# Optimization experiments

Measured on AMD Instinct MI355X. Metric: run time of the kernel, lower is better.

Reference implementation:

```python
import jax, jax.numpy as jnp
import numpy as np

B, C, L = 32, 64, 4096
HIDDEN = 64
SR = 50.0
KS = (7, 15, 31, 63)
PHYS = 12
EPS_BN = 1e-5
EPS_GN = 1e-5


def _dwconv(x, w):
    # x: (B,C,L), w: (C,1,k) depthwise kernel, SAME padding for odd k
    k = w.shape[-1]
    p = (k - 1) // 2
    return jax.lax.conv_general_dilated(
        x, w, window_strides=(1,), padding=[(p, p)],
        dimension_numbers=('NCH', 'OIH', 'NCH'),
        feature_group_count=x.shape[1])


def _physics(x):
    b, c, l = x.shape
    svm = jnp.sqrt((x * x).sum(axis=1))                      # (B,L) channel norm
    svm_max = svm.max(axis=-1)
    svm_mean = svm.mean(axis=-1)
    svm_std = jnp.std(svm, axis=-1, ddof=1) + 1e-6           # torch.std is unbiased
    jerk = jnp.diff(x, axis=-1) * SR                         # (B,C,L-1)
    jerk_max = jnp.abs(jerk).max(axis=-1).mean(axis=-1)      # (B,)
    jerk_rate = jnp.diff(jerk, axis=-1) * SR
    jerk_rate_max = jnp.abs(jerk_rate).max(axis=-1).mean(axis=-1)
    sign_changes = (x[:, :, :-1] * x[:, :, 1:] < 0).astype(x.dtype)
    zcr = sign_changes.sum(axis=-1).mean(axis=-1) / l
    thr = (svm_mean + 2.0 * svm_std)[:, None]
    impact_duration = (svm > thr).astype(x.dtype).sum(axis=-1) / l
    hthr = (svm_mean + 3.0 * svm_std)[:, None]
    impact_ratio = (svm > hthr).astype(x.dtype).sum(axis=-1) / l
    free_fall = (svm < (svm_mean - svm_std)[:, None]).astype(x.dtype).sum(axis=-1) / l
    second_half = svm[:, l // 2:]
    post_stillness = jnp.tanh(1.0 / (jnp.std(second_half, axis=-1, ddof=1) + 1e-6))
    third = max(1, l // 3)
    pre_mean = svm[:, :third].mean(axis=-1)
    impact_peak = svm[:, third:2 * third].max(axis=-1)
    post_mean = svm[:, 2 * third:].mean(axis=-1)
    fall_phase = jax.nn.relu(impact_peak - pre_mean) + jax.nn.relu(impact_peak - post_mean)
    fall_phase = fall_phase / (jnp.abs(impact_peak) + 1e-6)
    spectrum = jnp.fft.rfft(x.astype(jnp.float32), axis=-1, norm='ortho')
    power = (jnp.abs(spectrum) ** 2).sum(axis=1)             # (B, L//2+1)
    freqs = jnp.linspace(0.0, 1.0, power.shape[-1], dtype=power.dtype)
    total_power = power.sum(axis=-1) + 1e-6
    spectral_centroid = (power * freqs).sum(axis=-1) / total_power
    high_freq_ratio = jnp.where(freqs > 0.4, power, 0.0).sum(axis=-1) / total_power
    feats = jnp.stack([svm_max, svm_mean, jerk_max, jerk_rate_max, zcr,
                       impact_duration, impact_ratio, post_stillness, free_fall,
                       spectral_centroid, high_freq_ratio, fall_phase], axis=-1)
    return jnp.nan_to_num(feats, nan=0.0, posinf=0.0, neginf=0.0).astype(x.dtype)


def _forward(x, dw_w7, dw_w15, dw_w31, dw_w63, bn_g, bn_b, bn_m, bn_v,
             comp_w1, comp_b1, comp_w2, comp_b2,
             pn_g, pn_b, pn_m, pn_v,
             pe_w1, pe_b1, pe_w2, pe_b2, pg_w, pg_b,
             temperature, gn_g, gn_b, proj_w, proj_b, res_scale):
    # 4 depthwise conv + BN(eval) branches
    branches = []
    for i, w in enumerate((dw_w7, dw_w15, dw_w31, dw_w63)):
        y = _dwconv(x, w)
        y = (y - bn_m[i][None, :, None]) / jnp.sqrt(bn_v[i][None, :, None] + EPS_BN) \
            * bn_g[i][None, :, None] + bn_b[i][None, :, None]
        branches.append(y)
    stacked = jnp.stack(branches, axis=1)                    # (B,4,C,L)
    # complexity net: global avg pool -> MLP
    xm = x.mean(axis=-1)                                     # (B,C)
    h = jax.nn.relu(xm @ comp_w1 + comp_b1)
    complexity_logits = h @ comp_w2 + comp_b2                # (B,4)
    # physics gate
    pf = _physics(x)                                         # (B,12)
    pf = (pf - pn_m) / jnp.sqrt(pn_v + EPS_BN) * pn_g + pn_b
    pe = jax.nn.relu(jax.nn.relu(pf @ pe_w1 + pe_b1) @ pe_w2 + pe_b2)
    physics_weights = jax.nn.sigmoid(pe @ pg_w + pg_b)       # (B,4)
    temp = jnp.maximum(temperature, 0.1)
    weights = jax.nn.softmax(complexity_logits * physics_weights / temp, axis=-1)
    mixed = jnp.einsum('bkcl,bk->bcl', stacked, weights)
    # proj: GroupNorm(1,C) -> GELU(exact) -> 1x1 conv
    mu = mixed.mean(axis=(1, 2), keepdims=True)
    var = mixed.var(axis=(1, 2), keepdims=True)
    gn = (mixed - mu) / jnp.sqrt(var + EPS_GN) * gn_g[None, :, None] + gn_b[None, :, None]
    act = jax.nn.gelu(gn, approximate=False)
    out = jnp.einsum('oc,bcl->bol', proj_w, act) + proj_b[None, :, None]
    return x + res_scale * out


def setup_inputs() -> dict:
    ks = jax.random.split(jax.random.key(0), 16)
    f32 = jnp.float32
    inp = {}
    inp['x'] = jax.random.normal(ks[0], (B, C, L), dtype=f32)
    for i, k in enumerate(KS):
        inp[f'dw_w{k}'] = jax.random.normal(ks[1 + i], (C, 1, k), dtype=f32) / np.sqrt(k)
    inp['bn_g'] = jnp.ones((4, C), f32)
    inp['bn_b'] = jnp.zeros((4, C), f32)
    inp['bn_m'] = 0.1 * jax.random.normal(ks[5], (4, C), dtype=f32)
    inp['bn_v'] = jax.random.uniform(ks[6], (4, C), dtype=f32, minval=0.5, maxval=1.5)
    inp['comp_w1'] = jax.random.normal(ks[7], (C, HIDDEN), dtype=f32) / np.sqrt(C)
    inp['comp_b1'] = jnp.zeros((HIDDEN,), f32)
    inp['comp_w2'] = jax.random.normal(ks[8], (HIDDEN, 4), dtype=f32) / np.sqrt(HIDDEN)
    inp['comp_b2'] = jnp.zeros((4,), f32)
    inp['pn_g'] = jnp.ones((PHYS,), f32)
    inp['pn_b'] = jnp.zeros((PHYS,), f32)
    inp['pn_m'] = 0.1 * jax.random.normal(ks[9], (PHYS,), dtype=f32)
    inp['pn_v'] = jax.random.uniform(ks[10], (PHYS,), dtype=f32, minval=0.5, maxval=1.5)
    inp['pe_w1'] = jax.random.normal(ks[11], (PHYS, 32), dtype=f32) / np.sqrt(PHYS)
    inp['pe_b1'] = jnp.zeros((32,), f32)
    inp['pe_w2'] = jax.random.normal(ks[12], (32, 32), dtype=f32) / np.sqrt(32)
    inp['pe_b2'] = jnp.zeros((32,), f32)
    inp['pg_w'] = jax.random.normal(ks[13], (32, 4), dtype=f32) / np.sqrt(32)
    inp['pg_b'] = jnp.zeros((4,), f32)
    inp['temperature'] = jnp.asarray(1.0, f32)
    inp['gn_g'] = jnp.ones((C,), f32)
    inp['gn_b'] = jnp.zeros((C,), f32)
    inp['proj_w'] = jax.random.normal(ks[14], (C, C), dtype=f32) / np.sqrt(C)
    inp['proj_b'] = jnp.zeros((C,), f32)
    inp['res_scale'] = jnp.asarray(0.5, f32)  # init is 0.0; 0.5 gives a non-trivial output
    return inp


def reference(x, dw_w7, dw_w15, dw_w31, dw_w63, bn_g, bn_b, bn_m, bn_v,
              comp_w1, comp_b1, comp_w2, comp_b2,
              pn_g, pn_b, pn_m, pn_v,
              pe_w1, pe_b1, pe_w2, pe_b2, pg_w, pg_b,
              temperature, gn_g, gn_b, proj_w, proj_b, res_scale):
    return _forward(x, dw_w7, dw_w15, dw_w31, dw_w63, bn_g, bn_b, bn_m, bn_v,
                    comp_w1, comp_b1, comp_w2, comp_b2, pn_g, pn_b, pn_m, pn_v,
                    pe_w1, pe_b1, pe_w2, pe_b2, pg_w, pg_b,
                    temperature, gn_g, gn_b, proj_w, proj_b, res_scale)
```

## Files before the change

kernel.cpp:

```cpp
#include <hip/hip_runtime.h>
#include <math.h>

#define LN 4096
#define CN 64
#define BQ 32
#define NTH 256

#define OFF_CHAN_SUM    0
#define OFF_CHAN_JERK   2048
#define OFF_CHAN_JRATE  4096
#define OFF_CHAN_ZCR    6144
#define OFF_SVMST_PART  8192
#define OFF_SPEC_PART   12288
#define OFF_EFF_B       15360
#define OFF_GNP         17408
#define OFF_EFF_W       21504
#define OFF_SVMBUF      152576

#define FP(i) ((i) + ((i) >> 4))

__device__ __forceinline__ void bfly4(float2& a, float2& b, float2& c, float2& d,
                                      float w1r, float w1i, float w2r, float w2i,
                                      float w3r, float w3i) {
  float t1r = b.x*w1r - b.y*w1i, t1i = b.x*w1i + b.y*w1r;
  float t2r = c.x*w2r - c.y*w2i, t2i = c.x*w2i + c.y*w2r;
  float t3r = d.x*w3r - d.y*w3i, t3i = d.x*w3i + d.y*w3r;
  float ar = a.x + t2r, ai = a.y + t2i;
  float br = a.x - t2r, bi = a.y - t2i;
  float cr = t1r + t3r, ci = t1i + t3i;
  float dr = t1r - t3r, di = t1i - t3i;
  a = make_float2(ar + cr, ai + ci);
  b = make_float2(br + di, bi - dr);
  c = make_float2(ar - cr, ai - ci);
  d = make_float2(br - di, bi + dr);
}

__global__ __launch_bounds__(NTH) void kS(const float* __restrict__ x, float* __restrict__ ws) {
  __shared__ __align__(16) char smraw[34880];
  int role = blockIdx.x;
  int t = threadIdx.x;

  if (role < 2048) {
    int bc = role;
    const float* row = x + (size_t)bc * LN;
    int l0 = t * 16;
    float rd[18];
    const float4* r4 = (const float4*)(row + l0);
#pragma unroll
    for (int q = 0; q < 4; q++) {
      float4 v = r4[q];
      rd[4*q] = v.x; rd[4*q+1] = v.y; rd[4*q+2] = v.z; rd[4*q+3] = v.w;
    }
    if (t < 255) { rd[16] = row[l0 + 16]; rd[17] = row[l0 + 17]; }
    else { rd[16] = 0.f; rd[17] = 0.f; }
    float lsum = 0.f, jm = 0.f, jrm = 0.f; int zc = 0;
#pragma unroll
    for (int i = 0; i < 16; i++) {
      float a = rd[i], b2 = rd[i+1];
      lsum += a;
      int l = l0 + i;
      if (l < LN - 1) {
        jm = fmaxf(jm, fabsf(b2 - a));
        zc += (a * b2 < 0.f);
        if (l < LN - 2) jrm = fmaxf(jrm, fabsf(rd[i+2] - 2.f*b2 + a));
      }
    }
    for (int off = 32; off > 0; off >>= 1) {
      lsum += __shfl_down(lsum, off);
      jm = fmaxf(jm, __shfl_down(jm, off));
      jrm = fmaxf(jrm, __shfl_down(jrm, off));
      zc += __shfl_down(zc, off);
    }
    float* s1 = (float*)smraw; float* s2_ = s1 + 4; float* s3 = s1 + 8; int* s4 = (int*)(s1 + 12);
    int w = t >> 6;
    if ((t & 63) == 0) { s1[w] = lsum; s2_[w] = jm; s3[w] = jrm; s4[w] = zc; }
    __syncthreads();
    if (t == 0) {
      float S = 0, J = 0, JR = 0; int Z = 0;
      for (int i = 0; i < 4; i++) { S += s1[i]; J = fmaxf(J, s2_[i]); JR = fmaxf(JR, s3[i]); Z += s4[i]; }
      ws[OFF_CHAN_SUM + bc]   = S;
      ws[OFF_CHAN_JERK + bc]  = J * 50.f;
      ws[OFF_CHAN_JRATE + bc] = JR * 2500.f;
      ws[OFF_CHAN_ZCR + bc]   = (float)Z;
    }
  } else if (role < 2560) {
    int blk = role - 2048;
    int b = blk >> 4, lt = blk & 15;
    int l = lt * 256 + t;
    const float* xb = x + (size_t)b * CN * LN + l;
    float acc = 0.f;
#pragma unroll
    for (int c = 0; c < CN; c++) { float v = xb[(size_t)c * LN]; acc = fmaf(v, v, acc); }
    float svm = sqrtf(acc);
    ws[OFF_SVMBUF + (size_t)b * LN + l] = svm;
    const int third = LN / 3;
    float vS = svm, vS2 = svm * svm;
    float vS2H  = (l >= LN/2) ? svm : 0.f;
    float vS2H2 = (l >= LN/2) ? svm * svm : 0.f;
    float vPRE  = (l < third) ? svm : 0.f;
    float vPOST = (l >= 2*third) ? svm : 0.f;
    float vMX = svm;
    float vMID = (l >= third && l < 2*third) ? svm : 0.f;
    for (int off = 32; off > 0; off >>= 1) {
      vS += __shfl_down(vS, off); vS2 += __shfl_down(vS2, off);
      vS2H += __shfl_down(vS2H, off); vS2H2 += __shfl_down(vS2H2, off);
      vPRE += __shfl_down(vPRE, off); vPOST += __shfl_down(vPOST, off);
      vMX = fmaxf(vMX, __shfl_down(vMX, off));
      vMID = fmaxf(vMID, __shfl_down(vMID, off));
    }
    float (*red)[4] = (float(*)[4])smraw;
    int w = t >> 6;
    if ((t & 63) == 0) {
      red[0][w] = vS; red[1][w] = vS2; red[2][w] = vMX; red[3][w] = vS2H;
      red[4][w] = vS2H2; red[5][w] = vPRE; red[6][w] = vMID; red[7][w] = vPOST;
    }
    __syncthreads();
    if (t == 0) {
      float* sp = ws + OFF_SVMST_PART + (size_t)blk * 8;
      sp[0] = red[0][0]+red[0][1]+red[0][2]+red[0][3];
      sp[1] = red[1][0]+red[1][1]+red[1][2]+red[1][3];
      sp[2] = fmaxf(fmaxf(red[2][0],red[2][1]),fmaxf(red[2][2],red[2][3]));
      sp[3] = red[3][0]+red[3][1]+red[3][2]+red[3][3];
      sp[4] = red[4][0]+red[4][1]+red[4][2]+red[4][3];
      sp[5] = red[5][0]+red[5][1]+red[5][2]+red[5][3];
      sp[6] = fmaxf(fmaxf(red[6][0],red[6][1]),fmaxf(red[6][2],red[6][3]));
      sp[7] = red[7][0]+red[7][1]+red[7][2]+red[7][3];
    }
  } else {
    int blk = role - 2560;
    int b = blk >> 5, cp = blk & 31;
    const float* r0 = x + ((size_t)b * CN + 2 * cp) * LN;
    const float* r1 = r0 + LN;
    float2* z = (float2*)smraw;
    float (*red)[4] = (float(*)[4])(smraw + 34816);
#pragma unroll
    for (int k = 0; k < 4; k++) {
      int n4 = (k * 256 + t) * 4;
      float4 a = *(const float4*)(r0 + n4);
      float4 c = *(const float4*)(r1 + n4);
      float ar[4] = {a.x, a.y, a.z, a.w}, cr[4] = {c.x, c.y, c.z, c.w};
#pragma unroll
      for (int q = 0; q < 4; q++) {
        unsigned n = (unsigned)(n4 + q);
        unsigned br = __brev(n) >> 20;
        unsigned dr = ((br & 0x555u) << 1) | ((br & 0xAAAu) >> 1);
        z[FP(dr)] = make_float2(ar[q], cr[q]);
      }
    }
    __syncthreads();
    const float c8r[4] = { 1.f, 0.92387953251f, 0.70710678119f, 0.38268343236f };
    const float c8i[4] = { 0.f, -0.38268343236f, -0.70710678119f, -0.92387953251f };
#pragma unroll
    for (int p = 0; p < 3; p++) {
      const int H = (p == 0) ? 1 : (p == 1) ? 16 : 256;
      int r = t & (H - 1);
      int B = ((t / H) * 16 * H) + r;
      float2 E[16];
#pragma unroll
      for (int q = 0; q < 16; q++) E[q] = z[FP(B + q * H)];
      float su, cu;
      sincospif((float)r / (8.0f * (float)H), &su, &cu);
      float ur = cu, ui = -su;
      float u2r = ur*ur - ui*ui, u2i = 2.f*ur*ui;
      float w1r = u2r*u2r - u2i*u2i, w1i = 2.f*u2r*u2i;
      float w2r = w1r*w1r - w1i*w1i, w2i = 2.f*w1r*w1i;
      float w3r = w2r*w1r - w2i*w1i, w3i = w2r*w1i + w2i*w1r;
#pragma unroll
      for (int m = 0; m < 4; m++)
        bfly4(E[4*m], E[4*m+1], E[4*m+2], E[4*m+3], w1r, w1i, w2r, w2i, w3r, w3i);
#pragma unroll
      for (int m = 0; m < 4; m++) {
        float W1r = ur*c8r[m] - ui*c8i[m];
        float W1i = ur*c8i[m] + ui*c8r[m];
        float W2r = W1r*W1r - W1i*W1i, W2i = 2.f*W1r*W1i;
        float W3r = W2r*W1r - W2i*W1i, W3i = W2r*W1i + W2i*W1r;
        bfly4(E[m], E[m+4], E[m+8], E[m+12], W1r, W1i, W2r, W2i, W3r, W3i);
      }
#pragma unroll
      for (int q = 0; q < 16; q++) z[FP(B + q * H)] = E[q];
      __syncthreads();
    }
    float tot = 0.f, cen = 0.f, hi = 0.f;
    for (int k = t; k <= LN / 2; k += NTH) {
      float p;
      if (k == 0 || k == LN / 2) {
        float2 v = z[FP(k)];
        p = v.x * v.x + v.y * v.y;
      } else {
        float2 zk = z[FP(k)], zn = z[FP(LN - k)];
        float a1 = zk.x + zn.x, a2 = zk.y - zn.y, a3 = zk.y + zn.y, a4 = zk.x - zn.x;
        p = 0.25f * (a1*a1 + a2*a2 + a3*a3 + a4*a4);
      }
      p *= (1.0f / LN);
      tot += p;
      cen += p * ((float)k * (1.0f / (LN / 2)));
      if (k >= 820) hi += p;
    }
    for (int off = 32; off > 0; off >>= 1) {
      tot += __shfl_down(tot, off);
      cen += __shfl_down(cen, off);
      hi  += __shfl_down(hi, off);
    }
    int w = t >> 6;
    if ((t & 63) == 0) { red[0][w] = tot; red[1][w] = cen; red[2][w] = hi; }
    __syncthreads();
    if (t == 0) {
      float* sp = ws + OFF_SPEC_PART + (size_t)blk * 3;
      sp[0] = red[0][0]+red[0][1]+red[0][2]+red[0][3];
      sp[1] = red[1][0]+red[1][1]+red[1][2]+red[1][3];
      sp[2] = red[2][0]+red[2][1]+red[2][2]+red[2][3];
    }
  }
}

__global__ __launch_bounds__(NTH) void k4_gate(
    const float* __restrict__ dw7, const float* __restrict__ dw15,
    const float* __restrict__ dw31, const float* __restrict__ dw63,
    const float* __restrict__ bn_g, const float* __restrict__ bn_b,
    const float* __restrict__ bn_m, const float* __restrict__ bn_v,
    const float* __restrict__ comp_w1, const float* __restrict__ comp_b1,
    const float* __restrict__ comp_w2, const float* __restrict__ comp_b2,
    const float* __restrict__ pn_g, const float* __restrict__ pn_b,
    const float* __restrict__ pn_m, const float* __restrict__ pn_v,
    const float* __restrict__ pe_w1, const float* __restrict__ pe_b1,
    const float* __restrict__ pe_w2, const float* __restrict__ pe_b2,
    const float* __restrict__ pg_w, const float* __restrict__ pg_b,
    const float* __restrict__ temperature,
    float* __restrict__ ws)
{
  int b = blockIdx.x, t = threadIdx.x;
  __shared__ float sp8[16][8];
  __shared__ float sp3[32][3];
  __shared__ float stv[10];
  __shared__ float bc2[2];
  __shared__ float xm[64], h[64], pf[12], pe1v[32], pe2v[32], lgts[4], wts[4];
  __shared__ int ri[3][4], cnts[3];
  if (t < 16) {
    const float* p = ws + OFF_SVMST_PART + (size_t)(b * 16 + t) * 8;
#pragma unroll
    for (int i = 0; i < 8; i++) sp8[t][i] = p[i];
  }
  if (t >= 32 && t < 64) {
    int i = t - 32;
    const float* p = ws + OFF_SPEC_PART + (size_t)(b * 32 + i) * 3;
    sp3[i][0] = p[0]; sp3[i][1] = p[1]; sp3[i][2] = p[2];
  }
  __syncthreads();
  if (t == 0) {
    float S=0,S2=0,MX=-1e30f,S2H=0,S2H2=0,PRE=0,MID=-1e30f,POST=0;
    for (int i = 0; i < 16; i++) {
      S += sp8[i][0]; S2 += sp8[i][1]; MX = fmaxf(MX, sp8[i][2]);
      S2H += sp8[i][3]; S2H2 += sp8[i][4]; PRE += sp8[i][5];
      MID = fmaxf(MID, sp8[i][6]); POST += sp8[i][7];
    }
    float tot=0,cen=0,hi=0;
    for (int i = 0; i < 32; i++) { tot += sp3[i][0]; cen += sp3[i][1]; hi += sp3[i][2]; }
    stv[0]=S; stv[1]=S2; stv[2]=MX; stv[3]=S2H; stv[4]=S2H2;
    stv[5]=PRE; stv[6]=MID; stv[7]=POST; stv[8]=cen/(tot+1e-6f); stv[9]=hi/(tot+1e-6f);
    float mean = S * (1.f / LN);
    float var = (S2 - S * S * (1.f / LN)) * (1.f / (LN - 1));
    var = fmaxf(var, 0.f);
    bc2[0] = mean;
    bc2[1] = sqrtf(var) + 1e-6f;
  }
  __syncthreads();
  float mean = bc2[0], stde = bc2[1];
  float thr2 = mean + 2.f * stde, thr3 = mean + 3.f * stde, thrf = mean - stde;
  const float* svm = ws + OFF_SVMBUF + (size_t)b * LN;
  int c2 = 0, c3 = 0, cf = 0;
  for (int l = t; l < LN; l += NTH) {
    float v = svm[l];
    c2 += (v > thr2); c3 += (v > thr3); cf += (v < thrf);
  }
  for (int off = 32; off > 0; off >>= 1) {
    c2 += __shfl_down(c2, off); c3 += __shfl_down(c3, off); cf += __shfl_down(cf, off);
  }
  int w = t >> 6;
  if ((t & 63) == 0) { ri[0][w] = c2; ri[1][w] = c3; ri[2][w] = cf; }
  float j = 0.f, jr = 0.f, zz = 0.f;
  if (t < 64) {
    xm[t] = ws[OFF_CHAN_SUM + b * 64 + t] * (1.0f / LN);
    j  = ws[OFF_CHAN_JERK + b * 64 + t];
    jr = ws[OFF_CHAN_JRATE + b * 64 + t];
    zz = ws[OFF_CHAN_ZCR + b * 64 + t];
    for (int off = 32; off > 0; off >>= 1) {
      j += __shfl_down(j, off); jr += __shfl_down(jr, off); zz += __shfl_down(zz, off);
    }
  }
  __syncthreads();
  if (t == 0) {
    cnts[0] = ri[0][0]+ri[0][1]+ri[0][2]+ri[0][3];
    cnts[1] = ri[1][0]+ri[1][1]+ri[1][2]+ri[1][3];
    cnts[2] = ri[2][0]+ri[2][1]+ri[2][2]+ri[2][3];
    const int third = LN / 3;
    float S2H = stv[3], S2H2 = stv[4];
    float n2 = (float)(LN / 2);
    float var2 = (S2H2 - S2H * S2H / n2) / (n2 - 1.f);
    var2 = fmaxf(var2, 0.f);
    float post_still = tanhf(1.f / (sqrtf(var2) + 1e-6f));
    float pre_mean = stv[5] / (float)third;
    float post_mean = stv[7] / (float)(LN - 2 * third);
    float pk = stv[6];
    float fp = fmaxf(pk - pre_mean, 0.f) + fmaxf(pk - post_mean, 0.f);
    fp = fp / (fabsf(pk) + 1e-6f);
    pf[0] = stv[2];
    pf[1] = mean;
    pf[2] = j * (1.f / 64);
    pf[3] = jr * (1.f / 64);
    pf[4] = (zz * (1.f / 64)) * (1.f / LN);
    pf[5] = (float)cnts[0] / LN;
    pf[6] = (float)cnts[1] / LN;
    pf[7] = post_still;
    pf[8] = (float)cnts[2] / LN;
    pf[9] = stv[8];
    pf[10] = stv[9];
    pf[11] = fp;
  }
  __syncthreads();
  if (t < 12) pf[t] = (pf[t] - pn_m[t]) * rsqrtf(pn_v[t] + 1e-5f) * pn_g[t] + pn_b[t];
  __syncthreads();
  if (t < 64) {
    float hv = comp_b1[t];
    for (int i = 0; i < 64; i++) hv = fmaf(xm[i], comp_w1[i * 64 + t], hv);
    h[t] = fmaxf(hv, 0.f);
  }
  if (t < 32) {
    float v = pe_b1[t];
    for (int i = 0; i < 12; i++) v = fmaf(pf[i], pe_w1[i * 32 + t], v);
    pe1v[t] = fmaxf(v, 0.f);
  }
  __syncthreads();
  if (t < 32) {
    float v = pe_b2[t];
    for (int i = 0; i < 32; i++) v = fmaf(pe1v[i], pe_w2[i * 32 + t], v);
    pe2v[t] = fmaxf(v, 0.f);
  }
  __syncthreads();
  if (t < 4) {
    float v = comp_b2[t];
    for (int i = 0; i < 64; i++) v = fmaf(h[i], comp_w2[i * 4 + t], v);
    float g = pg_b[t];
    for (int i = 0; i < 32; i++) g = fmaf(pe2v[i], pg_w[i * 4 + t], g);
    g = 1.f / (1.f + expf(-g));
    float temp = fmaxf(temperature[0], 0.1f);
    lgts[t] = v * g / temp;
  }
  __syncthreads();
  if (t < 4) {
    float m = fmaxf(fmaxf(lgts[0], lgts[1]), fmaxf(lgts[2], lgts[3]));
    float den = expf(lgts[0]-m) + expf(lgts[1]-m) + expf(lgts[2]-m) + expf(lgts[3]-m);
    wts[t] = expf(lgts[t] - m) / den;
  }
  __syncthreads();
  if (t < 64) {
    int c = t;
    float w0 = wts[0], w1 = wts[1], w2 = wts[2], w3 = wts[3];
    float sc0 = bn_g[0*64+c] * rsqrtf(bn_v[0*64+c] + 1e-5f);
    float sc1 = bn_g[1*64+c] * rsqrtf(bn_v[1*64+c] + 1e-5f);
    float sc2 = bn_g[2*64+c] * rsqrtf(bn_v[2*64+c] + 1e-5f);
    float sc3 = bn_g[3*64+c] * rsqrtf(bn_v[3*64+c] + 1e-5f);
    float o0 = bn_b[0*64+c] - bn_m[0*64+c] * sc0;
    float o1 = bn_b[1*64+c] - bn_m[1*64+c] * sc1;
    float o2 = bn_b[2*64+c] - bn_m[2*64+c] * sc2;
    float o3 = bn_b[3*64+c] - bn_m[3*64+c] * sc3;
    ws[OFF_EFF_B + b * 64 + c] = w0*o0 + w1*o1 + w2*o2 + w3*o3;
    float a0 = w0*sc0, a1 = w1*sc1, a2 = w2*sc2, a3 = w3*sc3;
    float* eff = ws + OFF_EFF_W + (size_t)(b * 64 + c) * 64;
    for (int tau = 0; tau < 64; tau++) {
      float v = 0.f;
      if (tau < 63) {
        v = a3 * dw63[c * 63 + tau];
        int i7 = tau - 28;  if (i7 >= 0 && i7 < 7)   v = fmaf(a0, dw7[c * 7 + i7], v);
        int i15 = tau - 24; if (i15 >= 0 && i15 < 15) v = fmaf(a1, dw15[c * 15 + i15], v);
        int i31 = tau - 16; if (i31 >= 0 && i31 < 31) v = fmaf(a2, dw31[c * 31 + i31], v);
      }
      eff[tau] = v;
    }
  }
}

__device__ __forceinline__ float4 ldmask(const float* __restrict__ row, int idx) {
  int idxc = idx < 0 ? 0 : (idx > LN - 4 ? LN - 4 : idx);
  float4 v = *(const float4*)(row + idxc);
  float m = (idx == idxc) ? 1.f : 0.f;
  v.x *= m; v.y *= m; v.z *= m; v.w *= m;
  return v;
}

#define F16(wv,a0,a1,a2,a3,a4,a5,a6,a7,a8,a9,aA,aB,aC,aD,aE,aF) \
  acc[0]=fmaf(wv,a0,acc[0]);  acc[1]=fmaf(wv,a1,acc[1]);  acc[2]=fmaf(wv,a2,acc[2]);  acc[3]=fmaf(wv,a3,acc[3]);  \
  acc[4]=fmaf(wv,a4,acc[4]);  acc[5]=fmaf(wv,a5,acc[5]);  acc[6]=fmaf(wv,a6,acc[6]);  acc[7]=fmaf(wv,a7,acc[7]);  \
  acc[8]=fmaf(wv,a8,acc[8]);  acc[9]=fmaf(wv,a9,acc[9]);  acc[10]=fmaf(wv,aA,acc[10]); acc[11]=fmaf(wv,aB,acc[11]); \
  acc[12]=fmaf(wv,aC,acc[12]); acc[13]=fmaf(wv,aD,acc[13]); acc[14]=fmaf(wv,aE,acc[14]); acc[15]=fmaf(wv,aF,acc[15]);

__global__ __launch_bounds__(NTH) void k5_conv(const float* __restrict__ x,
                                               float* __restrict__ ws,
                                               float* __restrict__ mixed_out) {
  int bc = blockIdx.x;
  int t = threadIdx.x;
  __shared__ float wt[64];
  __shared__ float biasS;
  __shared__ double rda[2][4];
  if (t < 64) wt[t] = ws[OFF_EFF_W + (size_t)bc * 64 + t];
  if (t == 0) biasS = ws[OFF_EFF_B + bc];
  const float* row = x + (size_t)bc * LN;
  int l0 = t * 16;
  int g0 = l0 - 32;
  float4 R0 = ldmask(row, g0);
  float4 R1 = ldmask(row, g0 + 4);
  float4 R2 = ldmask(row, g0 + 8);
  float4 R3 = ldmask(row, g0 + 12);
  float4 R4 = ldmask(row, g0 + 16);
  __syncthreads();
  float bias = biasS;
  float acc[16];
#pragma unroll
  for (int jj = 0; jj < 16; jj++) acc[jj] = bias;
#pragma unroll
  for (int g = 0; g < 16; g++) {
    float w0 = wt[4*g], w1 = wt[4*g+1], w2 = wt[4*g+2], w3 = wt[4*g+3];
    F16(w0, R0.y,R0.z,R0.w,R1.x,R1.y,R1.z,R1.w,R2.x,R2.y,R2.z,R2.w,R3.x,R3.y,R3.z,R3.w,R4.x)
    F16(w1, R0.z,R0.w,R1.x,R1.y,R1.z,R1.w,R2.x,R2.y,R2.z,R2.w,R3.x,R3.y,R3.z,R3.w,R4.x,R4.y)
    F16(w2, R0.w,R1.x,R1.y,R1.z,R1.w,R2.x,R2.y,R2.z,R2.w,R3.x,R3.y,R3.z,R3.w,R4.x,R4.y,R4.z)
    F16(w3, R1.x,R1.y,R1.z,R1.w,R2.x,R2.y,R2.z,R2.w,R3.x,R3.y,R3.z,R3.w,R4.x,R4.y,R4.z,R4.w)
    if (g < 15) {
      R0 = R1; R1 = R2; R2 = R3; R3 = R4;
      R4 = ldmask(row, g0 + 4 * (g + 5));
    }
  }
  double ls = 0, ls2 = 0;
#pragma unroll
  for (int jj = 0; jj < 16; jj++) { float v = acc[jj]; ls += v; ls2 += (double)v * (double)v; }
  for (int off = 32; off > 0; off >>= 1) {
    ls += __shfl_down(ls, off);
    ls2 += __shfl_down(ls2, off);
  }
  int w = t >> 6;
  if ((t & 63) == 0) { rda[0][w] = ls; rda[1][w] = ls2; }
  __syncthreads();
  if (t == 0) {
    double* gp = (double*)(ws + OFF_GNP);
    gp[2 * bc + 0] = rda[0][0]+rda[0][1]+rda[0][2]+rda[0][3];
    gp[2 * bc + 1] = rda[1][0]+rda[1][1]+rda[1][2]+rda[1][3];
  }
  float* dst = mixed_out + (size_t)bc * LN + l0;
#pragma unroll
  for (int q = 0; q < 4; q++) {
    float4 v; v.x = acc[4*q]; v.y = acc[4*q+1]; v.z = acc[4*q+2]; v.w = acc[4*q+3];
    *(float4*)(dst + 4 * q) = v;
  }
}

__global__ __launch_bounds__(NTH) void k6_final(const float* __restrict__ x,
    const float* __restrict__ proj_w, const float* __restrict__ proj_b,
    const float* __restrict__ gn_g, const float* __restrict__ gn_b,
    const float* __restrict__ res_scale,
    const float* __restrict__ ws, float* out) {
  int blk = blockIdx.x;
  int b = blk >> 5;
  int l0 = (blk & 31) * 128;
  __shared__ float actS[64 * 128];
  __shared__ float Wt[64 * 64];
  __shared__ double rg[2][4];
  __shared__ float bcst[2];
  int t = threadIdx.x;
  {
    const double* gp = (const double*)(ws + OFF_GNP) + (size_t)b * CN * 2;
    double s1 = 0, s2 = 0;
    for (int i = t; i < CN; i += NTH) { s1 += gp[2*i]; s2 += gp[2*i+1]; }
    for (int off = 32; off > 0; off >>= 1) { s1 += __shfl_down(s1, off); s2 += __shfl_down(s2, off); }
    int w = t >> 6;
    if ((t & 63) == 0) { rg[0][w] = s1; rg[1][w] = s2; }
    __syncthreads();
    if (t == 0) {
      double S1 = rg[0][0]+rg[0][1]+rg[0][2]+rg[0][3];
      double S2 = rg[1][0]+rg[1][1]+rg[1][2]+rg[1][3];
      const double NN = 64.0 * 4096.0;
      double mud = S1 / NN;
      bcst[0] = (float)mud;
      bcst[1] = rsqrtf((float)(S2 / NN - mud * mud) + 1e-5f);
    }
  }
  for (int i = t; i < 4096; i += NTH) {
    int o = i & 63, c = i >> 6;
    Wt[c * 64 + o] = proj_w[o * 64 + c];
  }
  __syncthreads();
  float mu = bcst[0], rstd = bcst[1];
  const float* mx = out + (size_t)b * CN * LN;
  for (int i = t; i < 8192; i += NTH) {
    int c = i >> 7, l = i & 127;
    float v = mx[(size_t)c * LN + l0 + l];
    float g = (v - mu) * rstd * gn_g[c] + gn_b[c];
    float a = 0.5f * g * (1.f + erff(g * 0.70710678118654752f));
    actS[c * 128 + l] = a;
  }
  __syncthreads();
  int lg = t & 31;
  int og = (t >> 5) * 8;
  float4 acc4[8];
#pragma unroll
  for (int q = 0; q < 8; q++) { acc4[q].x = 0.f; acc4[q].y = 0.f; acc4[q].z = 0.f; acc4[q].w = 0.f; }
  for (int c = 0; c < 64; c++) {
    float4 a = *(const float4*)&actS[c * 128 + lg * 4];
    float4 wlo = *(const float4*)&Wt[c * 64 + og];
    float4 whi = *(const float4*)&Wt[c * 64 + og + 4];
    float wv[8] = { wlo.x, wlo.y, wlo.z, wlo.w, whi.x, whi.y, whi.z, whi.w };
#pragma unroll
    for (int q = 0; q < 8; q++) {
      acc4[q].x = fmaf(wv[q], a.x, acc4[q].x);
      acc4[q].y = fmaf(wv[q], a.y, acc4[q].y);
      acc4[q].z = fmaf(wv[q], a.z, acc4[q].z);
      acc4[q].w = fmaf(wv[q], a.w, acc4[q].w);
    }
  }
  float rsv = res_scale[0];
  const float* xb = x + (size_t)b * CN * LN;
  float* ob = out + (size_t)b * CN * LN;
#pragma unroll
  for (int q = 0; q < 8; q++) {
    int o = og + q;
    float pb = proj_b[o];
    size_t base = (size_t)o * LN + l0 + lg * 4;
    float4 xv = *(const float4*)&xb[base];
    float4 r;
    r.x = xv.x + rsv * (acc4[q].x + pb);
    r.y = xv.y + rsv * (acc4[q].y + pb);
    r.z = xv.z + rsv * (acc4[q].z + pb);
    r.w = xv.w + rsv * (acc4[q].w + pb);
    *(float4*)&ob[base] = r;
  }
}

extern "C" void kernel_launch(void* const* d_in, const int* in_sizes, int n_in,
                              void* d_out, int out_size, void* d_ws, size_t ws_size,
                              hipStream_t stream) {
  const float* x        = (const float*)d_in[0];
  const float* dw7      = (const float*)d_in[1];
  const float* dw15     = (const float*)d_in[2];
  const float* dw31     = (const float*)d_in[3];
  const float* dw63     = (const float*)d_in[4];
  const float* bn_g     = (const float*)d_in[5];
  const float* bn_b     = (const float*)d_in[6];
  const float* bn_m     = (const float*)d_in[7];
  const float* bn_v     = (const float*)d_in[8];
  const float* comp_w1  = (const float*)d_in[9];
  const float* comp_b1  = (const float*)d_in[10];
  const float* comp_w2  = (const float*)d_in[11];
  const float* comp_b2  = (const float*)d_in[12];
  const float* pn_g     = (const float*)d_in[13];
  const float* pn_b     = (const float*)d_in[14];
  const float* pn_m     = (const float*)d_in[15];
  const float* pn_v     = (const float*)d_in[16];
  const float* pe_w1    = (const float*)d_in[17];
  const float* pe_b1    = (const float*)d_in[18];
  const float* pe_w2    = (const float*)d_in[19];
  const float* pe_b2    = (const float*)d_in[20];
  const float* pg_w     = (const float*)d_in[21];
  const float* pg_b     = (const float*)d_in[22];
  const float* temperature = (const float*)d_in[23];
  const float* gn_g     = (const float*)d_in[24];
  const float* gn_b     = (const float*)d_in[25];
  const float* proj_w   = (const float*)d_in[26];
  const float* proj_b   = (const float*)d_in[27];
  const float* res_scale= (const float*)d_in[28];
  float* ws = (float*)d_ws;
  float* out = (float*)d_out;

  hipLaunchKernelGGL(kS, dim3(2048 + 512 + 1024), dim3(NTH), 0, stream, x, ws);
  hipLaunchKernelGGL(k4_gate, dim3(BQ), dim3(NTH), 0, stream,
                     dw7, dw15, dw31, dw63, bn_g, bn_b, bn_m, bn_v,
                     comp_w1, comp_b1, comp_w2, comp_b2,
                     pn_g, pn_b, pn_m, pn_v, pe_w1, pe_b1, pe_w2, pe_b2,
                     pg_w, pg_b, temperature, ws);
  hipLaunchKernelGGL(k5_conv, dim3(BQ * CN), dim3(NTH), 0, stream, x, ws, out);
  hipLaunchKernelGGL(k6_final, dim3(BQ * 32), dim3(NTH), 0, stream,
                     x, proj_w, proj_b, gn_g, gn_b, res_scale, ws, out);
}
```

Before: 240.7 us.

## Fuse gate computation into depthwise conv kernel and retile final projection

```diff
diff --git a/kernel.cpp b/kernel.cpp
--- a/kernel.cpp
+++ b/kernel.cpp
@@ -12,9 +12,7 @@
 #define OFF_CHAN_ZCR    6144
 #define OFF_SVMST_PART  8192
 #define OFF_SPEC_PART   12288
-#define OFF_EFF_B       15360
 #define OFF_GNP         17408
-#define OFF_EFF_W       21504
 #define OFF_SVMBUF      152576
 
 #define FP(i) ((i) + ((i) >> 4))
@@ -213,7 +211,22 @@
   }
 }
 
-__global__ __launch_bounds__(NTH) void k4_gate(
+__device__ __forceinline__ float4 ldmask(const float* __restrict__ row, int idx) {
+  int idxc = idx < 0 ? 0 : (idx > LN - 4 ? LN - 4 : idx);
+  float4 v = *(const float4*)(row + idxc);
+  float m = (idx == idxc) ? 1.f : 0.f;
+  v.x *= m; v.y *= m; v.z *= m; v.w *= m;
+  return v;
+}
+
+#define F16(wv,a0,a1,a2,a3,a4,a5,a6,a7,a8,a9,aA,aB,aC,aD,aE,aF) \
+  acc[0]=fmaf(wv,a0,acc[0]);  acc[1]=fmaf(wv,a1,acc[1]);  acc[2]=fmaf(wv,a2,acc[2]);  acc[3]=fmaf(wv,a3,acc[3]);  \
+  acc[4]=fmaf(wv,a4,acc[4]);  acc[5]=fmaf(wv,a5,acc[5]);  acc[6]=fmaf(wv,a6,acc[6]);  acc[7]=fmaf(wv,a7,acc[7]);  \
+  acc[8]=fmaf(wv,a8,acc[8]);  acc[9]=fmaf(wv,a9,acc[9]);  acc[10]=fmaf(wv,aA,acc[10]); acc[11]=fmaf(wv,aB,acc[11]); \
+  acc[12]=fmaf(wv,aC,acc[12]); acc[13]=fmaf(wv,aD,acc[13]); acc[14]=fmaf(wv,aE,acc[14]); acc[15]=fmaf(wv,aF,acc[15]);
+
+__global__ __launch_bounds__(NTH) void k5g(
+    const float* __restrict__ x,
     const float* __restrict__ dw7, const float* __restrict__ dw15,
     const float* __restrict__ dw31, const float* __restrict__ dw63,
     const float* __restrict__ bn_g, const float* __restrict__ bn_b,
@@ -226,15 +239,30 @@
     const float* __restrict__ pe_w2, const float* __restrict__ pe_b2,
     const float* __restrict__ pg_w, const float* __restrict__ pg_b,
     const float* __restrict__ temperature,
-    float* __restrict__ ws)
+    float* __restrict__ ws, float* __restrict__ mixed_out)
 {
-  int b = blockIdx.x, t = threadIdx.x;
+  int bc = blockIdx.x;
+  int b = bc >> 6, c = bc & 63;
+  int t = threadIdx.x;
   __shared__ float sp8[16][8];
   __shared__ float sp3[32][3];
   __shared__ float stv[10];
   __shared__ float bc2[2];
   __shared__ float xm[64], h[64], pf[12], pe1v[32], pe2v[32], lgts[4], wts[4];
   __shared__ int ri[3][4], cnts[3];
+  __shared__ float wt[64];
+  __shared__ float biasS;
+  __shared__ double rda[2][4];
+
+  const float* row = x + (size_t)bc * LN;
+  int l0 = t * 16;
+  int g0 = l0 - 32;
+  float4 R0 = ldmask(row, g0);
+  float4 R1 = ldmask(row, g0 + 4);
+  float4 R2 = ldmask(row, g0 + 8);
+  float4 R3 = ldmask(row, g0 + 12);
+  float4 R4 = ldmask(row, g0 + 16);
+
   if (t < 16) {
     const float* p = ws + OFF_SVMST_PART + (size_t)(b * 16 + t) * 8;
 #pragma unroll
@@ -353,64 +381,29 @@
   }
   __syncthreads();
   if (t < 64) {
-    int c = t;
     float w0 = wts[0], w1 = wts[1], w2 = wts[2], w3 = wts[3];
     float sc0 = bn_g[0*64+c] * rsqrtf(bn_v[0*64+c] + 1e-5f);
     float sc1 = bn_g[1*64+c] * rsqrtf(bn_v[1*64+c] + 1e-5f);
     float sc2 = bn_g[2*64+c] * rsqrtf(bn_v[2*64+c] + 1e-5f);
     float sc3 = bn_g[3*64+c] * rsqrtf(bn_v[3*64+c] + 1e-5f);
-    float o0 = bn_b[0*64+c] - bn_m[0*64+c] * sc0;
-    float o1 = bn_b[1*64+c] - bn_m[1*64+c] * sc1;
-    float o2 = bn_b[2*64+c] - bn_m[2*64+c] * sc2;
-    float o3 = bn_b[3*64+c] - bn_m[3*64+c] * sc3;
-    ws[OFF_EFF_B + b * 64 + c] = w0*o0 + w1*o1 + w2*o2 + w3*o3;
+    if (t == 0) {
+      float o0 = bn_b[0*64+c] - bn_m[0*64+c] * sc0;
+      float o1 = bn_b[1*64+c] - bn_m[1*64+c] * sc1;
+      float o2 = bn_b[2*64+c] - bn_m[2*64+c] * sc2;
+      float o3 = bn_b[3*64+c] - bn_m[3*64+c] * sc3;
+      biasS = wts[0]*o0 + wts[1]*o1 + wts[2]*o2 + wts[3]*o3;
+    }
     float a0 = w0*sc0, a1 = w1*sc1, a2 = w2*sc2, a3 = w3*sc3;
-    float* eff = ws + OFF_EFF_W + (size_t)(b * 64 + c) * 64;
-    for (int tau = 0; tau < 64; tau++) {
-      float v = 0.f;
-      if (tau < 63) {
-        v = a3 * dw63[c * 63 + tau];
-        int i7 = tau - 28;  if (i7 >= 0 && i7 < 7)   v = fmaf(a0, dw7[c * 7 + i7], v);
-        int i15 = tau - 24; if (i15 >= 0 && i15 < 15) v = fmaf(a1, dw15[c * 15 + i15], v);
-        int i31 = tau - 16; if (i31 >= 0 && i31 < 31) v = fmaf(a2, dw31[c * 31 + i31], v);
-      }
-      eff[tau] = v;
-    }
-  }
-}
-
-__device__ __forceinline__ float4 ldmask(const float* __restrict__ row, int idx) {
-  int idxc = idx < 0 ? 0 : (idx > LN - 4 ? LN - 4 : idx);
-  float4 v = *(const float4*)(row + idxc);
-  float m = (idx == idxc) ? 1.f : 0.f;
-  v.x *= m; v.y *= m; v.z *= m; v.w *= m;
-  return v;
-}
-
-#define F16(wv,a0,a1,a2,a3,a4,a5,a6,a7,a8,a9,aA,aB,aC,aD,aE,aF) \
-  acc[0]=fmaf(wv,a0,acc[0]);  acc[1]=fmaf(wv,a1,acc[1]);  acc[2]=fmaf(wv,a2,acc[2]);  acc[3]=fmaf(wv,a3,acc[3]);  \
-  acc[4]=fmaf(wv,a4,acc[4]);  acc[5]=fmaf(wv,a5,acc[5]);  acc[6]=fmaf(wv,a6,acc[6]);  acc[7]=fmaf(wv,a7,acc[7]);  \
-  acc[8]=fmaf(wv,a8,acc[8]);  acc[9]=fmaf(wv,a9,acc[9]);  acc[10]=fmaf(wv,aA,acc[10]); acc[11]=fmaf(wv,aB,acc[11]); \
-  acc[12]=fmaf(wv,aC,acc[12]); acc[13]=fmaf(wv,aD,acc[13]); acc[14]=fmaf(wv,aE,acc[14]); acc[15]=fmaf(wv,aF,acc[15]);
-
-__global__ __launch_bounds__(NTH) void k5_conv(const float* __restrict__ x,
-                                               float* __restrict__ ws,
-                                               float* __restrict__ mixed_out) {
-  int bc = blockIdx.x;
-  int t = threadIdx.x;
-  __shared__ float wt[64];
-  __shared__ float biasS;
-  __shared__ double rda[2][4];
-  if (t < 64) wt[t] = ws[OFF_EFF_W + (size_t)bc * 64 + t];
-  if (t == 0) biasS = ws[OFF_EFF_B + bc];
-  const float* row = x + (size_t)bc * LN;
-  int l0 = t * 16;
-  int g0 = l0 - 32;
-  float4 R0 = ldmask(row, g0);
-  float4 R1 = ldmask(row, g0 + 4);
-  float4 R2 = ldmask(row, g0 + 8);
-  float4 R3 = ldmask(row, g0 + 12);
-  float4 R4 = ldmask(row, g0 + 16);
+    int tau = t;
+    float v = 0.f;
+    if (tau < 63) {
+      v = a3 * dw63[c * 63 + tau];
+      int i7 = tau - 28;  if (i7 >= 0 && i7 < 7)   v = fmaf(a0, dw7[c * 7 + i7], v);
+      int i15 = tau - 24; if (i15 >= 0 && i15 < 15) v = fmaf(a1, dw15[c * 15 + i15], v);
+      int i31 = tau - 16; if (i31 >= 0 && i31 < 31) v = fmaf(a2, dw31[c * 31 + i31], v);
+    }
+    wt[tau] = v;
+  }
   __syncthreads();
   float bias = biasS;
   float acc[16];
@@ -435,7 +428,6 @@
     ls += __shfl_down(ls, off);
     ls2 += __shfl_down(ls2, off);
   }
-  int w = t >> 6;
   if ((t & 63) == 0) { rda[0][w] = ls; rda[1][w] = ls2; }
   __syncthreads();
   if (t == 0) {
@@ -457,9 +449,9 @@
     const float* __restrict__ res_scale,
     const float* __restrict__ ws, float* out) {
   int blk = blockIdx.x;
-  int b = blk >> 5;
-  int l0 = (blk & 31) * 128;
-  __shared__ float actS[64 * 128];
+  int b = blk >> 6;
+  int l0 = (blk & 63) * 64;
+  __shared__ float actS[64 * 64];
   __shared__ float Wt[64 * 64];
   __shared__ double rg[2][4];
   __shared__ float bcst[2];
@@ -482,32 +474,31 @@
     }
   }
   for (int i = t; i < 4096; i += NTH) {
-    int o = i & 63, c = i >> 6;
-    Wt[c * 64 + o] = proj_w[o * 64 + c];
+    int o = i & 63, cc = i >> 6;
+    Wt[cc * 64 + o] = proj_w[o * 64 + cc];
   }
   __syncthreads();
   float mu = bcst[0], rstd = bcst[1];
   const float* mx = out + (size_t)b * CN * LN;
-  for (int i = t; i < 8192; i += NTH) {
-    int c = i >> 7, l = i & 127;
-    float v = mx[(size_t)c * LN + l0 + l];
-    float g = (v - mu) * rstd * gn_g[c] + gn_b[c];
+  for (int i = t; i < 4096; i += NTH) {
+    int cc = i >> 6, l = i & 63;
+    float v = mx[(size_t)cc * LN + l0 + l];
+    float g = (v - mu) * rstd * gn_g[cc] + gn_b[cc];
     float a = 0.5f * g * (1.f + erff(g * 0.70710678118654752f));
-    actS[c * 128 + l] = a;
-  }
-  __syncthreads();
-  int lg = t & 31;
-  int og = (t >> 5) * 8;
-  float4 acc4[8];
-#pragma unroll
-  for (int q = 0; q < 8; q++) { acc4[q].x = 0.f; acc4[q].y = 0.f; acc4[q].z = 0.f; acc4[q].w = 0.f; }
-  for (int c = 0; c < 64; c++) {
-    float4 a = *(const float4*)&actS[c * 128 + lg * 4];
-    float4 wlo = *(const float4*)&Wt[c * 64 + og];
-    float4 whi = *(const float4*)&Wt[c * 64 + og + 4];
-    float wv[8] = { wlo.x, wlo.y, wlo.z, wlo.w, whi.x, whi.y, whi.z, whi.w };
-#pragma unroll
-    for (int q = 0; q < 8; q++) {
+    actS[cc * 64 + l] = a;
+  }
+  __syncthreads();
+  int lg = t & 15;
+  int og = (t >> 4) * 4;
+  float4 acc4[4];
+#pragma unroll
+  for (int q = 0; q < 4; q++) { acc4[q].x = 0.f; acc4[q].y = 0.f; acc4[q].z = 0.f; acc4[q].w = 0.f; }
+  for (int cc = 0; cc < 64; cc++) {
+    float4 a = *(const float4*)&actS[cc * 64 + lg * 4];
+    float4 wv4 = *(const float4*)&Wt[cc * 64 + og];
+    float wv[4] = { wv4.x, wv4.y, wv4.z, wv4.w };
+#pragma unroll
+    for (int q = 0; q < 4; q++) {
       acc4[q].x = fmaf(wv[q], a.x, acc4[q].x);
       acc4[q].y = fmaf(wv[q], a.y, acc4[q].y);
       acc4[q].z = fmaf(wv[q], a.z, acc4[q].z);
@@ -518,7 +509,7 @@
   const float* xb = x + (size_t)b * CN * LN;
   float* ob = out + (size_t)b * CN * LN;
 #pragma unroll
-  for (int q = 0; q < 8; q++) {
+  for (int q = 0; q < 4; q++) {
     int o = og + q;
     float pb = proj_b[o];
     size_t base = (size_t)o * LN + l0 + lg * 4;
@@ -568,12 +559,11 @@
   float* out = (float*)d_out;
 
   hipLaunchKernelGGL(kS, dim3(2048 + 512 + 1024), dim3(NTH), 0, stream, x, ws);
-  hipLaunchKernelGGL(k4_gate, dim3(BQ), dim3(NTH), 0, stream,
-                     dw7, dw15, dw31, dw63, bn_g, bn_b, bn_m, bn_v,
+  hipLaunchKernelGGL(k5g, dim3(BQ * CN), dim3(NTH), 0, stream,
+                     x, dw7, dw15, dw31, dw63, bn_g, bn_b, bn_m, bn_v,
                      comp_w1, comp_b1, comp_w2, comp_b2,
                      pn_g, pn_b, pn_m, pn_v, pe_w1, pe_b1, pe_w2, pe_b2,
-                     pg_w, pg_b, temperature, ws);
-  hipLaunchKernelGGL(k5_conv, dim3(BQ * CN), dim3(NTH), 0, stream, x, ws, out);
-  hipLaunchKernelGGL(k6_final, dim3(BQ * 32), dim3(NTH), 0, stream,
+                     pg_w, pg_b, temperature, ws, out);
+  hipLaunchKernelGGL(k6_final, dim3(BQ * 64), dim3(NTH), 0, stream,
                      x, proj_w, proj_b, gn_g, gn_b, res_scale, ws, out);
 }
```

Measured after the change: 251.0 us. 4.3% more time.
